# Kernel tuning notes

Measured on AMD Instinct MI355X. Metric: run time of the kernel, lower is better.

## Reference

```python
import jax, jax.numpy as jnp
import numpy as np

B, N, C = 4, 4096, 16
HID, OUT = 64, 64
ALL_K, K = 128, 32          # k + k_pos = 32
KD, KDP = 8, 6              # k_dilated, k_dilated_pos
EPS = 1e-5
NEG_SLOPE = 0.2


def setup_inputs() -> dict:
    ks = jax.random.split(jax.random.key(0), 12)
    C2, C4 = 2 * C, 4 * C
    return {
        "x": jax.random.normal(ks[0], (B, N, C), jnp.float32),
        "pos": jax.random.normal(ks[1], (B, N, 3), jnp.float32),
        "W1": jax.random.normal(ks[2], (C2, C2), jnp.float32) * 0.1,
        "g1": jnp.ones((C2,), jnp.float32),
        "b1": jnp.zeros((C2,), jnp.float32),
        "W2": jax.random.normal(ks[3], (HID, C4), jnp.float32) * 0.05,
        "g2": jnp.ones((HID,), jnp.float32),
        "b2": jnp.zeros((HID,), jnp.float32),
        "W3": jax.random.normal(ks[4], (OUT, HID), jnp.float32) * 0.05,
        "g3": jnp.ones((OUT,), jnp.float32),
        "b3": jnp.zeros((OUT,), jnp.float32),
    }


def pdist2(a):
    # squared pairwise distances (same top-k ordering as cdist p=2, and
    # avoids sqrt(0) on the diagonal). a: (B,N,D) -> (B,N,N)
    sq = jnp.sum(a * a, axis=-1)
    d = sq[:, :, None] + sq[:, None, :] - 2.0 * jnp.einsum('bnd,bmd->bnm', a, a)
    return jnp.maximum(d, 0.0)


def knn_excl_self(d2, k):
    # k nearest excluding self (self is the unique 0-distance nearest point)
    idx = jax.lax.top_k(-d2, k + 1)[1]
    return idx[..., 1:]


def fps(pts, npoint):
    # pts: (M, Kn, 3). Deterministic start at index 0 (torch version uses a
    # random start; only the sampled index set differs, math is identical).
    M, Kn, _ = pts.shape
    rows = jnp.arange(M)

    def body(i, state):
        centroids, distance, farthest = state
        centroids = centroids.at[:, i].set(farthest)
        centroid = pts[rows, farthest][:, None, :]            # (M,1,3)
        dist = jnp.sum((pts - centroid) ** 2, axis=-1)         # (M,Kn)
        distance = jnp.minimum(distance, dist)
        farthest = jnp.argmax(distance, axis=-1).astype(jnp.int32)
        return centroids, distance, farthest

    init = (jnp.zeros((M, npoint), jnp.int32),
            jnp.full((M, Kn), 1e10, jnp.float32),
            jnp.zeros((M,), jnp.int32))
    centroids, _, _ = jax.lax.fori_loop(0, npoint, body, init)
    return centroids


def edge_feat(feat, idx):
    # feat: (B,N,D) node features, idx: (B,N,Kn) neighbor indices
    # returns cat(neighbor - center, center): (B,N,Kn,2D)  (edge_function 249)
    nbr = feat[jnp.arange(feat.shape[0])[:, None, None], idx]  # (B,N,Kn,D)
    ctr = feat[:, :, None, :]
    return jnp.concatenate([nbr - ctr, jnp.broadcast_to(ctr, nbr.shape)], axis=-1)


def bn_lrelu(h, g, b):
    # BatchNorm2d with track_running_stats=False -> always batch stats.
    # h: (B,N,Kn,Cc), stats over (B,N,Kn) per channel.
    mu = jnp.mean(h, axis=(0, 1, 2), keepdims=True)
    var = jnp.var(h, axis=(0, 1, 2), keepdims=True)
    h = (h - mu) * jax.lax.rsqrt(var + EPS) * g + b
    return jnp.where(h > 0, h, NEG_SLOPE * h)


def reference(x, pos, W1, g1, b1, W2, g2, b2, W3, g3, b3):
    # --- dilated neighborhood: all_k nearest by position, FPS down to k ---
    cd2 = pdist2(pos)                                   # (B,N,N)
    idx_l = jax.lax.top_k(-cd2, ALL_K)[1]               # (B,N,ALL_K) incl. self
    idx_l_flat = idx_l.reshape(B * N, ALL_K)
    pts = pos.reshape(B * N, 3)[idx_l_flat]             # (B*N, ALL_K, 3)
    idx_fps_local = fps(pts, K)                         # (B*N, K)
    idx_fps = jnp.take_along_axis(idx_l_flat, idx_fps_local, axis=1)
    idx_fps = idx_fps.reshape(B, N, K)                  # (B,N,K)

    # --- dual kNN graph: k_dilated by feature distance + k_dilated_pos by pos ---
    idx_feat = knn_excl_self(pdist2(x), KD)             # (B,N,KD)
    idx_pos = knn_excl_self(cd2, KDP)                   # (B,N,KDP)
    idx1 = jnp.concatenate([idx_feat, idx_pos], axis=2)  # (B,N,KD+KDP)

    # --- conv1x1-BN-LeakyReLU on dual-graph edge features, max over nbrs ---
    e1 = edge_feat(x, idx1)                             # (B,N,14,2C)
    h1 = bn_lrelu(jnp.einsum('bnkc,oc->bnko', e1, W1), g1, b1)
    f1 = jnp.max(h1, axis=2)                            # (B,N,2C)

    # --- edge features on FPS-dilated graph, two conv1x1-BN-LeakyReLU ---
    e2 = edge_feat(f1, idx_fps)                         # (B,N,K,4C)
    h2 = bn_lrelu(jnp.einsum('bnkc,hc->bnkh', e2, W2), g2, b2)
    h3 = bn_lrelu(jnp.einsum('bnkh,oh->bnko', h2, W3), g3, b3)
    out = jnp.max(h3, axis=2)                           # (B,N,OUT)
    return out, idx1
```

## Files before the change

kernel.cpp:

```cpp
#include <hip/hip_runtime.h>

#define NPTS 4096
#define BNROWS 16384

__device__ __forceinline__ float lrelu(float h) { return h > 0.f ? h : 0.2f * h; }

#define WSYNC asm volatile("s_waitcnt lgkmcnt(0)" ::: "memory")

__device__ __forceinline__ float rfl(float v) {
  return __int_as_float(__builtin_amdgcn_readfirstlane(__float_as_int(v)));
}

__device__ __forceinline__ unsigned long long shflx64(unsigned long long v, int m) {
  int lo = __shfl_xor((int)(unsigned int)(v & 0xffffffffull), m, 64);
  int hi = __shfl_xor((int)(unsigned int)(v >> 32), m, 64);
  return ((unsigned long long)(unsigned int)hi << 32) | (unsigned int)lo;
}

__global__ __launch_bounds__(256) void norms_kernel(
    const float* __restrict__ x, float* __restrict__ sqx)
{
  int r = blockIdx.x * 256 + threadIdx.x;
  const float4* xp = (const float4*)(x + (size_t)r * 16);
  float4 a0 = xp[0], a1 = xp[1], a2 = xp[2], a3 = xp[3];
  float s = a0.x*a0.x + a0.y*a0.y + a0.z*a0.z + a0.w*a0.w
          + a1.x*a1.x + a1.y*a1.y + a1.z*a1.z + a1.w*a1.w
          + a2.x*a2.x + a2.y*a2.y + a2.z*a2.z + a2.w*a2.w
          + a3.x*a3.x + a3.y*a3.y + a3.z*a3.z + a3.w*a3.w;
  sqx[r] = s;
}

__global__ __launch_bounds__(512) void knn_pos_kernel(
    const float* __restrict__ pos, int* __restrict__ idx_l,
    int* __restrict__ idx1_i, float* __restrict__ idx1_f)
{
  __shared__ int cand[8][512];
  __shared__ unsigned int cCnt[8];
  int tid = threadIdx.x;
  int w = tid >> 6, lane = tid & 63;
  int r = blockIdx.x * 8 + w;
  int b = r >> 12, n = r & 4095;
  const float* pb = pos + (size_t)b * NPTS * 3;
  float cx = pb[n*3+0], cy = pb[n*3+1], cz = pb[n*3+2];
  if (lane == 0) cCnt[w] = 0u;
  WSYNC;

  unsigned int qp[32];
  int m1 = 65536, m2 = 65536, m3 = 65536;
  #pragma unroll
  for (int t = 0; t < 32; ++t) {
    unsigned int wq = 0u;
    #pragma unroll
    for (int h = 0; h < 2; ++h) {
      int j = (2*t + h) * 64 + lane;
      float dx = cx - pb[j*3+0], dy = cy - pb[j*3+1], dz = cz - pb[j*3+2];
      float d2 = dx*dx + dy*dy + dz*dz;
      int q = (int)(d2 * 1000.0f);
      q = q < 0 ? 0 : (q > 65535 ? 65535 : q);
      wq |= ((unsigned int)q) << (16*h);
      int nm1 = min(m1, q);
      int nm2 = min(m2, max(m1, q));
      int nm3 = min(m3, max(m2, q));
      m1 = nm1; m2 = nm2; m3 = nm3;
    }
    qp[t] = wq;
  }
  int lo = 0, hi = 65535;
  #pragma unroll
  for (int it = 0; it < 16; ++it) {
    int mid = (lo + hi) >> 1;
    int cnt = __popcll(__ballot(m3 <= mid));
    if (cnt >= 43) hi = mid; else lo = mid + 1;
  }
  unsigned int qt = (unsigned int)lo + 2u;

  #pragma unroll
  for (int t = 0; t < 32; ++t) {
    unsigned int wq = qp[t];
    unsigned int q0 = wq & 0xffffu, q1 = wq >> 16;
    if (q0 <= qt) { unsigned int p = atomicAdd(&cCnt[w], 1u); if (p < 512u) cand[w][p] = (2*t)*64 + lane; }
    if (q1 <= qt) { unsigned int p = atomicAdd(&cCnt[w], 1u); if (p < 512u) cand[w][p] = (2*t+1)*64 + lane; }
  }
  WSYNC;
  unsigned int nc = cCnt[w]; if (nc > 512u) nc = 512u;

  double cxd = (double)cx, cyd = (double)cy, czd = (double)cz;
  unsigned long long key[8];
  #pragma unroll
  for (int t = 0; t < 8; ++t) {
    int c = (t << 6) | lane;
    unsigned long long kk = ~0ull;
    if (c < (int)nc) {
      int id = cand[w][c];
      double dx = cxd - (double)pb[id*3+0];
      double dy = cyd - (double)pb[id*3+1];
      double dz = czd - (double)pb[id*3+2];
      double d2 = dx*dx + dy*dy + dz*dz;
      unsigned long long bits = (unsigned long long)__double_as_longlong(d2);
      kk = (bits & ~0xFFFull) | (unsigned long long)(unsigned int)id;
    }
    key[t] = kk;
  }

  #pragma unroll
  for (int kk2 = 1; kk2 <= 9; ++kk2) {
    const int k = 1 << kk2;
    #pragma unroll
    for (int jj = kk2 - 1; jj >= 0; --jj) {
      const int j = 1 << jj;
      if (j >= 64) {
        const int jt = j >> 6;
        #pragma unroll
        for (int t = 0; t < 8; ++t) {
          const int tp = t ^ jt;
          if (tp > t) {
            const bool up = (((t << 6) & k) == 0);
            unsigned long long a = key[t], bq = key[tp];
            if ((a > bq) == up) { key[t] = bq; key[tp] = a; }
          }
        }
      } else {
        #pragma unroll
        for (int t = 0; t < 8; ++t) {
          unsigned long long p = shflx64(key[t], j);
          bool up = ((((t << 6) | lane) & k) == 0);
          bool lower = ((lane & j) == 0);
          unsigned long long mn = (key[t] < p) ? key[t] : p;
          unsigned long long mx = (key[t] < p) ? p : key[t];
          key[t] = (lower == up) ? mn : mx;
        }
      }
    }
  }

  idx_l[(size_t)r * 128 + lane]      = (int)(key[0] & 0xFFFull);
  idx_l[(size_t)r * 128 + lane + 64] = (int)(key[1] & 0xFFFull);
  if (lane >= 1 && lane < 7) {
    int v = (int)(key[0] & 0xFFFull);
    idx1_i[r * 14 + 8 + (lane - 1)] = v;
    idx1_f[r * 14 + 8 + (lane - 1)] = (float)v;
  }
}

__global__ __launch_bounds__(256) void knn_feat_kernel(
    const float* __restrict__ x, const float* __restrict__ sqx,
    int* __restrict__ idx1_i, float* __restrict__ idx1_f)
{
  __shared__ float lmin[4][256];
  __shared__ int cand[4][192];
  __shared__ unsigned int cCnt[4];
  __shared__ float qtS[4];
  __shared__ float ctrf[4][16];
  int tid = threadIdx.x;
  int w = tid >> 6, lane = tid & 63;
  int rbase = blockIdx.x * 4;
  int b = rbase >> 12;
  const float* xb = x + (size_t)b * NPTS * 16;
  const float* sqb = sqx + b * NPTS;

  if (tid < 64) {
    int rr = tid >> 4, c = tid & 15;
    ctrf[rr][c] = xb[(size_t)((rbase + rr) & 4095) * 16 + c];
  }
  if (tid < 4) cCnt[tid] = 0u;
  __syncthreads();

  float cm[4][16], c2[4];
  #pragma unroll
  for (int rr = 0; rr < 4; ++rr) {
    float s = 0.f;
    #pragma unroll
    for (int c = 0; c < 16; ++c) {
      float v = ctrf[rr][c];
      cm[rr][c] = rfl(-2.0f * v);
      s = fmaf(v, v, s);
    }
    c2[rr] = rfl(s);
  }

  float key[4][16];
  float fk[4] = {3.4e38f, 3.4e38f, 3.4e38f, 3.4e38f};
  #pragma unroll
  for (int pt = 0; pt < 16; ++pt) {
    int j = tid + 256 * pt;
    const float4* xj = (const float4*)(xb + (size_t)j * 16);
    float4 a0 = xj[0], a1 = xj[1], a2 = xj[2], a3 = xj[3];
    float sqj = sqb[j];
    float va[16] = {a0.x,a0.y,a0.z,a0.w, a1.x,a1.y,a1.z,a1.w,
                    a2.x,a2.y,a2.z,a2.w, a3.x,a3.y,a3.z,a3.w};
    #pragma unroll
    for (int rr = 0; rr < 4; ++rr) {
      float acc = sqj + c2[rr];
      #pragma unroll
      for (int c = 0; c < 16; ++c) acc = fmaf(va[c], cm[rr][c], acc);
      key[rr][pt] = acc;
      fk[rr] = fminf(fk[rr], acc);
    }
  }
  #pragma unroll
  for (int rr = 0; rr < 4; ++rr) lmin[rr][tid] = fk[rr];
  __syncthreads();

  {
    float lv0 = lmin[w][lane], lv1 = lmin[w][lane + 64];
    float lv2 = lmin[w][lane + 128], lv3 = lmin[w][lane + 192];
    unsigned int lo = 0u, hi = 0x7F800000u;
    for (int it = 0; it < 31; ++it) {
      unsigned int mid = (lo + hi) >> 1;
      float midf = __uint_as_float(mid);
      int cnt = __popcll(__ballot(lv0 <= midf)) + __popcll(__ballot(lv1 <= midf))
              + __popcll(__ballot(lv2 <= midf)) + __popcll(__ballot(lv3 <= midf));
      if (cnt >= 10) hi = mid; else lo = mid + 1;
    }
    if (lane == 0) qtS[w] = __uint_as_float(hi) * 1.0002f + 1e-3f;
  }
  __syncthreads();

  {
    float q0 = qtS[0], q1 = qtS[1], q2 = qtS[2], q3 = qtS[3];
    #pragma unroll
    for (int pt = 0; pt < 16; ++pt) {
      int j = tid + 256 * pt;
      if (key[0][pt] <= q0) { unsigned int p = atomicAdd(&cCnt[0], 1u); if (p < 192u) cand[0][p] = j; }
      if (key[1][pt] <= q1) { unsigned int p = atomicAdd(&cCnt[1], 1u); if (p < 192u) cand[1][p] = j; }
      if (key[2][pt] <= q2) { unsigned int p = atomicAdd(&cCnt[2], 1u); if (p < 192u) cand[2][p] = j; }
      if (key[3][pt] <= q3) { unsigned int p = atomicAdd(&cCnt[3], 1u); if (p < 192u) cand[3][p] = j; }
    }
  }
  __syncthreads();

  {
    int nc = (int)cCnt[w]; if (nc > 192) nc = 192;
    double key64[3]; int kid[3];
    #pragma unroll
    for (int s = 0; s < 3; ++s) {
      int c = lane + 64*s;
      if (c < nc) {
        int id = cand[w][c];
        const float4* xp = (const float4*)(xb + (size_t)id * 16);
        float4 q0 = xp[0], q1 = xp[1], q2 = xp[2], q3 = xp[3];
        float xv[16] = {q0.x,q0.y,q0.z,q0.w, q1.x,q1.y,q1.z,q1.w,
                        q2.x,q2.y,q2.z,q2.w, q3.x,q3.y,q3.z,q3.w};
        double acc = 0.0;
        #pragma unroll
        for (int c2i = 0; c2i < 16; ++c2i) { double d = (double)ctrf[w][c2i] - (double)xv[c2i]; acc += d * d; }
        key64[s] = acc; kid[s] = id;
      } else { key64[s] = 1e300; kid[s] = 0x7fffffff; }
    }
    int row = rbase + w;
    for (int it = 0; it < 9; ++it) {
      double bk = key64[0]; int bi = kid[0], bs = 0;
      if (key64[1] < bk || (key64[1] == bk && kid[1] < bi)) { bk = key64[1]; bi = kid[1]; bs = 1; }
      if (key64[2] < bk || (key64[2] == bk && kid[2] < bi)) { bk = key64[2]; bi = kid[2]; bs = 2; }
      double rk = bk; int ri = bi;
      #pragma unroll
      for (int off = 32; off > 0; off >>= 1) {
        double ok = __shfl_xor(rk, off, 64);
        int oi = __shfl_xor(ri, off, 64);
        if (ok < rk || (ok == rk && oi < ri)) { rk = ok; ri = oi; }
      }
      if (it > 0 && lane == 0) {
        idx1_i[row * 14 + it - 1] = ri;
        idx1_f[row * 14 + it - 1] = (float)ri;
      }
      if (bi == ri) key64[bs] = 1e300;
    }
  }
}

__global__ __launch_bounds__(256) void fps_kernel(
    const float* __restrict__ pos, const int* __restrict__ idx_l, int* __restrict__ idx_fps)
{
  int wave = threadIdx.x >> 6, lane = threadIdx.x & 63;
  int r = blockIdx.x * 4 + wave;
  const int* il = idx_l + (size_t)r * 128;
  int gi0 = il[lane], gi1 = il[lane + 64];
  double x0 = (double)pos[gi0*3+0], y0 = (double)pos[gi0*3+1], z0 = (double)pos[gi0*3+2];
  double x1 = (double)pos[gi1*3+0], y1 = (double)pos[gi1*3+1], z1 = (double)pos[gi1*3+2];
  double d0 = 1e10, d1 = 1e10;
  int far = 0;
  int* outp = idx_fps + (size_t)r * 32;
  for (int i = 0; i < 32; ++i) {
    int ownerLane = far & 63;
    int sel = far >> 6;
    int gsel = sel ? gi1 : gi0;
    int gout = __shfl(gsel, ownerLane, 64);
    if (lane == 0) outp[i] = gout;
    double cx = __shfl(sel ? x1 : x0, ownerLane, 64);
    double cy = __shfl(sel ? y1 : y0, ownerLane, 64);
    double cz = __shfl(sel ? z1 : z0, ownerLane, 64);
    double t0 = (x0-cx)*(x0-cx) + (y0-cy)*(y0-cy) + (z0-cz)*(z0-cz);
    double t1 = (x1-cx)*(x1-cx) + (y1-cy)*(y1-cy) + (z1-cz)*(z1-cz);
    d0 = fmin(d0, t0); d1 = fmin(d1, t1);
    double v; int p;
    if (d1 > d0) { v = d1; p = lane + 64; } else { v = d0; p = lane; }
    for (int off = 32; off > 0; off >>= 1) {
      double ov = __shfl_xor(v, off, 64);
      int op = __shfl_xor(p, off, 64);
      if (ov > v || (ov == v && op < p)) { v = ov; p = op; }
    }
    far = p;
  }
}

__global__ __launch_bounds__(256) void sv_kernel(
    const float* __restrict__ x, const float* __restrict__ W1,
    float* __restrict__ s, float* __restrict__ v)
{
  __shared__ float xs[8][16];
  __shared__ float w1t[512], w1dt[512];
  int tid = threadIdx.x;
  int rbase = blockIdx.x * 8;
  for (int i = tid; i < 512; i += 256) {
    int c = i >> 5, o = i & 31;
    float a = W1[o * 32 + c], bb = W1[o * 32 + 16 + c];
    w1t[i] = a; w1dt[i] = bb - a;
  }
  if (tid < 128) { int rr = tid >> 4, c = tid & 15; xs[rr][c] = x[(size_t)(rbase + rr) * 16 + c]; }
  __syncthreads();
  int rr = tid >> 5, o = tid & 31;
  float sa = 0.f, va = 0.f;
  #pragma unroll
  for (int c = 0; c < 16; ++c) {
    float xv = xs[rr][c];
    sa = fmaf(xv, w1t[c * 32 + o], sa);
    va = fmaf(xv, w1dt[c * 32 + o], va);
  }
  int r = rbase + rr;
  s[(size_t)r * 32 + o] = sa;
  v[(size_t)r * 32 + o] = va;
}

__global__ __launch_bounds__(256) void h1stats_kernel(
    const float* __restrict__ s, const float* __restrict__ v, const int* __restrict__ idx1_i,
    double* __restrict__ slotsH1, float* __restrict__ h1max)
{
  __shared__ int sidx[8][14];
  __shared__ float sred[256], sred2[256];
  int tid = threadIdx.x;
  int rr = tid >> 5, o = tid & 31;
  int rbase = blockIdx.x * 8;
  if (tid < 112) { int q = tid / 14, k = tid % 14; sidx[q][k] = idx1_i[(rbase + q) * 14 + k]; }
  __syncthreads();
  int r = rbase + rr;
  int broff = r & ~4095;
  float vv = v[(size_t)r * 32 + o];
  float m = -3.4e38f, ls = 0.f, lss = 0.f;
  #pragma unroll
  for (int k = 0; k < 14; ++k) {
    int j = sidx[rr][k];
    float val = s[(size_t)(broff + j) * 32 + o] + vv;
    m = fmaxf(m, val);
    ls += val; lss += val * val;
  }
  h1max[(size_t)r * 32 + o] = m;
  sred[tid] = ls; sred2[tid] = lss;
  __syncthreads();
  if (tid < 32) {
    float s2 = 0.f, ss = 0.f;
    #pragma unroll
    for (int j = 0; j < 8; ++j) { s2 += sred[j * 32 + tid]; ss += sred2[j * 32 + tid]; }
    int slot = blockIdx.x & 255;
    atomicAdd(&slotsH1[slot * 64 + tid], (double)s2);
    atomicAdd(&slotsH1[slot * 64 + 32 + tid], (double)ss);
  }
}

__global__ void finalize_stats_kernel(const double* __restrict__ slots, int C, double cnt,
    const float* __restrict__ g, const float* __restrict__ bta, float* __restrict__ scsh)
{
  int o = threadIdx.x;
  if (o < C) {
    double s = 0.0, ss = 0.0;
    for (int slot = 0; slot < 256; ++slot) { s += slots[slot * 2 * C + o]; ss += slots[slot * 2 * C + C + o]; }
    double mu = s / cnt;
    double var = ss / cnt - mu * mu;
    double rs = 1.0 / sqrt(var + 1e-5);
    float sc = (float)rs * g[o];
    float sh = bta[o] - (float)mu * sc;
    scsh[o] = sc;
    scsh[C + o] = sh;
  }
}

__global__ __launch_bounds__(256) void tu_kernel(
    const float* __restrict__ h1max, const float* __restrict__ scsh1, const float* __restrict__ W2,
    float* __restrict__ t, float* __restrict__ u)
{
  __shared__ float f1s[4][32];
  __shared__ float w2t[2048], w2dt[2048];
  int tid = threadIdx.x;
  int rbase = blockIdx.x * 4;
  for (int i = tid; i < 2048; i += 256) {
    int c = i >> 6, o = i & 63;
    float a = W2[o * 64 + c], bb = W2[o * 64 + 32 + c];
    w2t[i] = a; w2dt[i] = bb - a;
  }
  if (tid < 128) {
    int rr = tid >> 5, c = tid & 31;
    f1s[rr][c] = lrelu(h1max[(size_t)(rbase + rr) * 32 + c] * scsh1[c] + scsh1[32 + c]);
  }
  __syncthreads();
  int rr = tid >> 6, o = tid & 63;
  float ta = 0.f, ua = 0.f;
  #pragma unroll
  for (int c = 0; c < 32; ++c) {
    float fv = f1s[rr][c];
    ta = fmaf(fv, w2t[c * 64 + o], ta);
    ua = fmaf(fv, w2dt[c * 64 + o], ua);
  }
  int r = rbase + rr;
  t[(size_t)r * 64 + o] = ta;
  u[(size_t)r * 64 + o] = ua;
}

__global__ __launch_bounds__(256) void h2stats_kernel(
    const float* __restrict__ t, const float* __restrict__ u, const int* __restrict__ idx_fps,
    double* __restrict__ slotsH2)
{
  __shared__ int nids[8][32];
  __shared__ float sred[256], sred2[256];
  int tid = threadIdx.x;
  int o = tid & 63, wv = tid >> 6;
  int rbase = blockIdx.x * 8;
  { int q = tid >> 5, k = tid & 31; nids[q][k] = idx_fps[(rbase + q) * 32 + k]; }
  __syncthreads();
  float ls = 0.f, lss = 0.f;
  for (int rr = 0; rr < 8; ++rr) {
    int r = rbase + rr;
    int broff = r & ~4095;
    float uo = u[(size_t)r * 64 + o];
    #pragma unroll
    for (int i = 0; i < 8; ++i) {
      int k = wv + 4 * i;
      float val = t[(size_t)(broff + nids[rr][k]) * 64 + o] + uo;
      ls += val; lss += val * val;
    }
  }
  sred[tid] = ls; sred2[tid] = lss;
  __syncthreads();
  if (tid < 64) {
    float s2 = sred[tid] + sred[tid + 64] + sred[tid + 128] + sred[tid + 192];
    float ss = sred2[tid] + sred2[tid + 64] + sred2[tid + 128] + sred2[tid + 192];
    int slot = blockIdx.x & 255;
    atomicAdd(&slotsH2[slot * 128 + tid], (double)s2);
    atomicAdd(&slotsH2[slot * 128 + 64 + tid], (double)ss);
  }
}

#define ROWS3 8
__global__ __launch_bounds__(256, 4) void h3_kernel(
    const float* __restrict__ t, const float* __restrict__ u, const int* __restrict__ idx_fps,
    const float* __restrict__ W3, const float* __restrict__ scsh2,
    double* __restrict__ slotsH3, float* __restrict__ h3max)
{
  __shared__ float h2lds[2048];
  __shared__ float wmax[256];
  __shared__ float sred[256], sred2[256];
  __shared__ int nids[ROWS3][32];
  int tid = threadIdx.x;
  int o = tid & 63, wv = tid >> 6;
  float4 w3r[16];
  const float4* w3p = (const float4*)(W3 + o * 64);
  #pragma unroll
  for (int j = 0; j < 16; ++j) w3r[j] = w3p[j];
  float sc2o = scsh2[o], sh2o = scsh2[64 + o];
  int rbase = blockIdx.x * ROWS3;
  { int q = tid >> 5, k = tid & 31; nids[q][k] = idx_fps[(rbase + q) * 32 + k]; }
  float ls = 0.f, lss = 0.f;
  __syncthreads();
  for (int rr = 0; rr < ROWS3; ++rr) {
    int r = rbase + rr;
    int broff = r & ~4095;
    float uo = u[(size_t)r * 64 + o];
    #pragma unroll
    for (int i = 0; i < 8; ++i) {
      int k = wv + 4 * i;
      float val = t[(size_t)(broff + nids[rr][k]) * 64 + o] + uo;
      h2lds[k * 64 + o] = lrelu(val * sc2o + sh2o);
    }
    __syncthreads();
    float kmax = -3.4e38f;
    #pragma unroll
    for (int i = 0; i < 8; ++i) {
      int k = wv + 4 * i;
      const float4* hp = (const float4*)(h2lds + k * 64);
      float acc = 0.f;
      #pragma unroll
      for (int j = 0; j < 16; ++j) {
        float4 h = hp[j];
        acc = fmaf(h.x, w3r[j].x, acc); acc = fmaf(h.y, w3r[j].y, acc);
        acc = fmaf(h.z, w3r[j].z, acc); acc = fmaf(h.w, w3r[j].w, acc);
      }
      ls += acc; lss += acc * acc;
      kmax = fmaxf(kmax, acc);
    }
    wmax[tid] = kmax;
    __syncthreads();
    if (tid < 64) {
      float m = fmaxf(fmaxf(wmax[tid], wmax[64 + tid]), fmaxf(wmax[128 + tid], wmax[192 + tid]));
      h3max[(size_t)r * 64 + tid] = m;
    }
  }
  sred[tid] = ls; sred2[tid] = lss;
  __syncthreads();
  if (tid < 64) {
    float s2 = sred[tid] + sred[tid + 64] + sred[tid + 128] + sred[tid + 192];
    float ss = sred2[tid] + sred2[tid + 64] + sred2[tid + 128] + sred2[tid + 192];
    int slot = blockIdx.x & 255;
    atomicAdd(&slotsH3[slot * 128 + tid], (double)s2);
    atomicAdd(&slotsH3[slot * 128 + 64 + tid], (double)ss);
  }
}

__global__ void out_kernel(const float* __restrict__ h3max, const float* __restrict__ scsh3,
                           float* __restrict__ out)
{
  int i = blockIdx.x * 256 + threadIdx.x;
  int o = i & 63;
  out[i] = lrelu(h3max[i] * scsh3[o] + scsh3[64 + o]);
}

extern "C" void kernel_launch(void* const* d_in, const int* in_sizes, int n_in,
                              void* d_out, int out_size, void* d_ws, size_t ws_size,
                              hipStream_t stream) {
  (void)in_sizes; (void)n_in; (void)out_size; (void)ws_size;
  const float* x   = (const float*)d_in[0];
  const float* pos = (const float*)d_in[1];
  const float* W1  = (const float*)d_in[2];
  const float* g1  = (const float*)d_in[3];
  const float* b1  = (const float*)d_in[4];
  const float* W2  = (const float*)d_in[5];
  const float* g2  = (const float*)d_in[6];
  const float* b2  = (const float*)d_in[7];
  const float* W3  = (const float*)d_in[8];
  const float* g3  = (const float*)d_in[9];
  const float* b3  = (const float*)d_in[10];

  float* out      = (float*)d_out;
  float* out_idx1 = out + 1048576;

  char* ws = (char*)d_ws;
  double* slotsH1 = (double*)(ws + 0);
  double* slotsH2 = (double*)(ws + 131072);
  double* slotsH3 = (double*)(ws + 393216);
  float*  scsh1   = (float*)(ws + 655360);
  float*  scsh2   = (float*)(ws + 655616);
  float*  scsh3   = (float*)(ws + 656128);
  float*  sqx     = (float*)(ws + 786432);
  int*    idx_l   = (int*)(ws + 1048576);
  float*  t_buf   = (float*)(ws + 1048576);
  float*  u_buf   = (float*)(ws + 5242880);
  int*    idx_fps = (int*)(ws + 9437184);
  int*    idx1_i  = (int*)(ws + 11534336);
  float*  h1max   = (float*)(ws + 12451840);
  float*  s_buf   = (float*)(ws + 14548992);
  float*  v_buf   = (float*)(ws + 16646144);
  float*  h3max   = (float*)(ws + 18743296);

  hipMemsetAsync(d_ws, 0, 656640, stream);

  norms_kernel   <<<dim3(64),   dim3(256), 0, stream>>>(x, sqx);
  knn_pos_kernel <<<dim3(2048), dim3(512), 0, stream>>>(pos, idx_l, idx1_i, out_idx1);
  knn_feat_kernel<<<dim3(4096), dim3(256), 0, stream>>>(x, sqx, idx1_i, out_idx1);
  fps_kernel     <<<dim3(4096), dim3(256), 0, stream>>>(pos, idx_l, idx_fps);
  sv_kernel      <<<dim3(2048), dim3(256), 0, stream>>>(x, W1, s_buf, v_buf);
  h1stats_kernel <<<dim3(2048), dim3(256), 0, stream>>>(s_buf, v_buf, idx1_i, slotsH1, h1max);
  finalize_stats_kernel<<<dim3(1), dim3(64), 0, stream>>>(slotsH1, 32, 229376.0, g1, b1, scsh1);
  tu_kernel      <<<dim3(4096), dim3(256), 0, stream>>>(h1max, scsh1, W2, t_buf, u_buf);
  h2stats_kernel <<<dim3(2048), dim3(256), 0, stream>>>(t_buf, u_buf, idx_fps, slotsH2);
  finalize_stats_kernel<<<dim3(1), dim3(64), 0, stream>>>(slotsH2, 64, 524288.0, g2, b2, scsh2);
  h3_kernel      <<<dim3(2048), dim3(256), 0, stream>>>(t_buf, u_buf, idx_fps, W3, scsh2, slotsH3, h3max);
  finalize_stats_kernel<<<dim3(1), dim3(64), 0, stream>>>(slotsH3, 64, 524288.0, g3, b3, scsh3);
  out_kernel     <<<dim3(4096), dim3(256), 0, stream>>>(h3max, scsh3, out);
}
```

Measured before the change: 666.1 us.

## Process 8 query rows per block in feature kNN with LDS-staged point tiles

The feature-distance kNN kernel now handles 8 query rows per 512-thread block instead of 4 per 256-thread block. It halves the number of blocks that each stream all 4096 points of the batch. Point features are staged cooperatively into a padded shared-memory tile with coalesced float4 loads, and each thread reads its point from LDS to compute 8 distances. This cuts redundant global reads of x and raises arithmetic reuse per load. In exchange it adds more registers per thread (8x16 centroid weights, an 8x8 key array), extra syncthreads per tile, and possibly lower occupancy.

```diff
diff --git a/kernel.cpp b/kernel.cpp
--- a/kernel.cpp
+++ b/kernel.cpp
@@ -6,10 +6,6 @@
 __device__ __forceinline__ float lrelu(float h) { return h > 0.f ? h : 0.2f * h; }
 
 #define WSYNC asm volatile("s_waitcnt lgkmcnt(0)" ::: "memory")
-
-__device__ __forceinline__ float rfl(float v) {
-  return __int_as_float(__builtin_amdgcn_readfirstlane(__float_as_int(v)));
-}
 
 __device__ __forceinline__ unsigned long long shflx64(unsigned long long v, int m) {
   int lo = __shfl_xor((int)(unsigned int)(v & 0xffffffffull), m, 64);
@@ -142,74 +138,96 @@
   }
 }
 
-__global__ __launch_bounds__(256) void knn_feat_kernel(
+#define FT_PAD 17
+__global__ __launch_bounds__(512) void knn_feat_kernel(
     const float* __restrict__ x, const float* __restrict__ sqx,
     int* __restrict__ idx1_i, float* __restrict__ idx1_f)
 {
-  __shared__ float lmin[4][256];
-  __shared__ int cand[4][192];
-  __shared__ unsigned int cCnt[4];
-  __shared__ float qtS[4];
-  __shared__ float ctrf[4][16];
+  __shared__ float tile[512 * FT_PAD];
+  __shared__ float lmin[8][512];
+  __shared__ int cand[8][192];
+  __shared__ unsigned int cCnt[8];
+  __shared__ float qtS[8];
+  __shared__ float ctrf[8][16];
   int tid = threadIdx.x;
   int w = tid >> 6, lane = tid & 63;
-  int rbase = blockIdx.x * 4;
+  int rbase = blockIdx.x * 8;
   int b = rbase >> 12;
   const float* xb = x + (size_t)b * NPTS * 16;
   const float* sqb = sqx + b * NPTS;
 
-  if (tid < 64) {
+  if (tid < 128) {
     int rr = tid >> 4, c = tid & 15;
     ctrf[rr][c] = xb[(size_t)((rbase + rr) & 4095) * 16 + c];
   }
-  if (tid < 4) cCnt[tid] = 0u;
-  __syncthreads();
-
-  float cm[4][16], c2[4];
-  #pragma unroll
-  for (int rr = 0; rr < 4; ++rr) {
+  if (tid < 8) cCnt[tid] = 0u;
+  __syncthreads();
+
+  float cm[8][16], c2[8];
+  #pragma unroll
+  for (int rr = 0; rr < 8; ++rr) {
     float s = 0.f;
     #pragma unroll
     for (int c = 0; c < 16; ++c) {
       float v = ctrf[rr][c];
-      cm[rr][c] = rfl(-2.0f * v);
+      cm[rr][c] = -2.0f * v;
       s = fmaf(v, v, s);
     }
-    c2[rr] = rfl(s);
-  }
-
-  float key[4][16];
-  float fk[4] = {3.4e38f, 3.4e38f, 3.4e38f, 3.4e38f};
-  #pragma unroll
-  for (int pt = 0; pt < 16; ++pt) {
-    int j = tid + 256 * pt;
-    const float4* xj = (const float4*)(xb + (size_t)j * 16);
-    float4 a0 = xj[0], a1 = xj[1], a2 = xj[2], a3 = xj[3];
+    c2[rr] = s;
+  }
+
+  float key[8][8];
+  float fk[8];
+  #pragma unroll
+  for (int rr = 0; rr < 8; ++rr) fk[rr] = 3.4e38f;
+
+  const float4* xb4 = (const float4*)xb;
+  #pragma unroll
+  for (int tb = 0; tb < 8; ++tb) {
+    __syncthreads();
+    #pragma unroll
+    for (int q = 0; q < 4; ++q) {
+      int f = q * 512 + tid;
+      int p = f >> 2, part = f & 3;
+      float4 v = xb4[tb * 2048 + f];
+      tile[p * FT_PAD + part * 4 + 0] = v.x;
+      tile[p * FT_PAD + part * 4 + 1] = v.y;
+      tile[p * FT_PAD + part * 4 + 2] = v.z;
+      tile[p * FT_PAD + part * 4 + 3] = v.w;
+    }
+    __syncthreads();
+    int j = tb * 512 + tid;
     float sqj = sqb[j];
-    float va[16] = {a0.x,a0.y,a0.z,a0.w, a1.x,a1.y,a1.z,a1.w,
-                    a2.x,a2.y,a2.z,a2.w, a3.x,a3.y,a3.z,a3.w};
-    #pragma unroll
-    for (int rr = 0; rr < 4; ++rr) {
-      float acc = sqj + c2[rr];
+    float acc[8];
+    #pragma unroll
+    for (int rr = 0; rr < 8; ++rr) acc[rr] = sqj + c2[rr];
+    #pragma unroll
+    for (int c = 0; c < 16; ++c) {
+      float va = tile[tid * FT_PAD + c];
       #pragma unroll
-      for (int c = 0; c < 16; ++c) acc = fmaf(va[c], cm[rr][c], acc);
-      key[rr][pt] = acc;
-      fk[rr] = fminf(fk[rr], acc);
-    }
-  }
-  #pragma unroll
-  for (int rr = 0; rr < 4; ++rr) lmin[rr][tid] = fk[rr];
+      for (int rr = 0; rr < 8; ++rr) acc[rr] = fmaf(va, cm[rr][c], acc[rr]);
+    }
+    #pragma unroll
+    for (int rr = 0; rr < 8; ++rr) {
+      key[rr][tb] = acc[rr];
+      fk[rr] = fminf(fk[rr], acc[rr]);
+    }
+  }
+  #pragma unroll
+  for (int rr = 0; rr < 8; ++rr) lmin[rr][tid] = fk[rr];
   __syncthreads();
 
   {
-    float lv0 = lmin[w][lane], lv1 = lmin[w][lane + 64];
-    float lv2 = lmin[w][lane + 128], lv3 = lmin[w][lane + 192];
+    float lv[8];
+    #pragma unroll
+    for (int t = 0; t < 8; ++t) lv[t] = lmin[w][lane + 64 * t];
     unsigned int lo = 0u, hi = 0x7F800000u;
     for (int it = 0; it < 31; ++it) {
       unsigned int mid = (lo + hi) >> 1;
       float midf = __uint_as_float(mid);
-      int cnt = __popcll(__ballot(lv0 <= midf)) + __popcll(__ballot(lv1 <= midf))
-              + __popcll(__ballot(lv2 <= midf)) + __popcll(__ballot(lv3 <= midf));
+      int cnt = 0;
+      #pragma unroll
+      for (int t = 0; t < 8; ++t) cnt += __popcll(__ballot(lv[t] <= midf));
       if (cnt >= 10) hi = mid; else lo = mid + 1;
     }
     if (lane == 0) qtS[w] = __uint_as_float(hi) * 1.0002f + 1e-3f;
@@ -217,14 +235,18 @@
   __syncthreads();
 
   {
-    float q0 = qtS[0], q1 = qtS[1], q2 = qtS[2], q3 = qtS[3];
-    #pragma unroll
-    for (int pt = 0; pt < 16; ++pt) {
-      int j = tid + 256 * pt;
-      if (key[0][pt] <= q0) { unsigned int p = atomicAdd(&cCnt[0], 1u); if (p < 192u) cand[0][p] = j; }
-      if (key[1][pt] <= q1) { unsigned int p = atomicAdd(&cCnt[1], 1u); if (p < 192u) cand[1][p] = j; }
-      if (key[2][pt] <= q2) { unsigned int p = atomicAdd(&cCnt[2], 1u); if (p < 192u) cand[2][p] = j; }
-      if (key[3][pt] <= q3) { unsigned int p = atomicAdd(&cCnt[3], 1u); if (p < 192u) cand[3][p] = j; }
+    float qr[8];
+    #pragma unroll
+    for (int rr = 0; rr < 8; ++rr) qr[rr] = qtS[rr];
+    #pragma unroll
+    for (int rr = 0; rr < 8; ++rr) {
+      #pragma unroll
+      for (int tb = 0; tb < 8; ++tb) {
+        if (key[rr][tb] <= qr[rr]) {
+          unsigned int p = atomicAdd(&cCnt[rr], 1u);
+          if (p < 192u) cand[rr][p] = tb * 512 + tid;
+        }
+      }
     }
   }
   __syncthreads();
@@ -562,7 +584,7 @@
 
   norms_kernel   <<<dim3(64),   dim3(256), 0, stream>>>(x, sqx);
   knn_pos_kernel <<<dim3(2048), dim3(512), 0, stream>>>(pos, idx_l, idx1_i, out_idx1);
-  knn_feat_kernel<<<dim3(4096), dim3(256), 0, stream>>>(x, sqx, idx1_i, out_idx1);
+  knn_feat_kernel<<<dim3(2048), dim3(512), 0, stream>>>(x, sqx, idx1_i, out_idx1);
   fps_kernel     <<<dim3(4096), dim3(256), 0, stream>>>(pos, idx_l, idx_fps);
   sv_kernel      <<<dim3(2048), dim3(256), 0, stream>>>(x, W1, s_buf, v_buf);
   h1stats_kernel <<<dim3(2048), dim3(256), 0, stream>>>(s_buf, v_buf, idx1_i, slotsH1, h1max);
```

New measurement: 686.6 us. 3.1% more time.
